# Optimization experiments

Hardware: AMD Instinct MI355X
Metric: run time of the kernel (lower is better)

The kernel has to match this reference:

```python
import jax, jax.numpy as jnp
import numpy as np

NUM_NODES = 50000
NUM_EDGES = 800000
INPUT_DIM = 256
OUTPUT_DIM = 256
NUM_HEADS = 8
HEAD_DIM = OUTPUT_DIM // NUM_HEADS


def setup_inputs() -> dict:
    key = jax.random.key(0)
    ks = jax.random.split(key, 14)
    x = jax.random.normal(ks[0], (NUM_NODES, INPUT_DIM), dtype=jnp.float32)
    edge_index = jax.random.randint(ks[1], (2, NUM_EDGES), 0, NUM_NODES, dtype=jnp.int32)
    # timestamps in seconds over ~11.5 days so log1p(|dt|/3600) is informative
    edge_time = jax.random.uniform(ks[2], (NUM_EDGES,), dtype=jnp.float32) * 1e6
    node_time = jax.random.uniform(ks[3], (NUM_NODES,), dtype=jnp.float32) * 1e6
    s_in = 1.0 / np.sqrt(INPUT_DIM)
    s_out = 1.0 / np.sqrt(OUTPUT_DIM)
    s_t = 1.0 / np.sqrt(2.0)
    Wq = jax.random.uniform(ks[4], (INPUT_DIM, OUTPUT_DIM), jnp.float32, -s_in, s_in)
    bq = jax.random.uniform(ks[5], (OUTPUT_DIM,), jnp.float32, -s_in, s_in)
    Wk = jax.random.uniform(ks[6], (INPUT_DIM, OUTPUT_DIM), jnp.float32, -s_in, s_in)
    bk = jax.random.uniform(ks[7], (OUTPUT_DIM,), jnp.float32, -s_in, s_in)
    Wv = jax.random.uniform(ks[8], (INPUT_DIM, OUTPUT_DIM), jnp.float32, -s_in, s_in)
    bv = jax.random.uniform(ks[9], (OUTPUT_DIM,), jnp.float32, -s_in, s_in)
    Wt = jax.random.uniform(ks[10], (2, NUM_HEADS), jnp.float32, -s_t, s_t)
    bt = jax.random.uniform(ks[11], (NUM_HEADS,), jnp.float32, -s_t, s_t)
    Wo = jax.random.uniform(ks[12], (OUTPUT_DIM, OUTPUT_DIM), jnp.float32, -s_out, s_out)
    bo = jax.random.uniform(ks[13], (OUTPUT_DIM,), jnp.float32, -s_out, s_out)
    return {"x": x, "edge_index": edge_index, "edge_time": edge_time, "node_time": node_time,
            "Wq": Wq, "bq": bq, "Wk": Wk, "bk": bk, "Wv": Wv, "bv": bv,
            "Wt": Wt, "bt": bt, "Wo": Wo, "bo": bo}


def reference(x, edge_index, edge_time, node_time, Wq, bq, Wk, bk, Wv, bv, Wt, bt, Wo, bo):
    n = x.shape[0]
    q = (x @ Wq + bq).reshape(n, NUM_HEADS, HEAD_DIM)
    k = (x @ Wk + bk).reshape(n, NUM_HEADS, HEAD_DIM)
    v = (x @ Wv + bv).reshape(n, NUM_HEADS, HEAD_DIM)
    src, dst = edge_index[0], edge_index[1]
    # temporal features per edge
    time_diff = edge_time - node_time[dst]
    time_features = jnp.stack(
        [jnp.sign(time_diff), jnp.log1p(jnp.abs(time_diff) / 3600.0)], axis=-1)  # [E, 2]
    temporal_weights = time_features @ Wt + bt  # [E, H]
    scale = HEAD_DIM ** -0.5
    scores = jnp.einsum('ehd,ehd->eh', q[dst], k[src]) * scale + temporal_weights  # [E, H]
    # softmax over ALL edges per head (dim=0), as in the original
    alpha = jax.nn.softmax(scores, axis=0)  # [E, H]
    msg = alpha[..., None] * v[src]  # [E, H, D]
    out = jax.ops.segment_sum(msg, dst, num_segments=n)  # [N, H, D]
    out = out.reshape(n, OUTPUT_DIM)
    return out @ Wo + bo
```

## Files before the change

kernel.cpp:

```cpp
#include <hip/hip_runtime.h>
#include <hip/hip_bf16.h>

#define NUM_NODES 50000
#define NUM_EDGES 800000
#define NUM_HEADS 8
#define HEAD_DIM 32
#define SCAN_BLOCKS 49

typedef unsigned short ushort8 __attribute__((ext_vector_type(8)));
typedef float f32x4 __attribute__((ext_vector_type(4)));
typedef __bf16 bf16x8 __attribute__((ext_vector_type(8)));

union BF8 { ushort8 u; bf16x8 b; };

__device__ __forceinline__ unsigned float_to_key(float f) {
    int i = __float_as_int(f);
    return (i >= 0) ? ((unsigned)i | 0x80000000u) : ~(unsigned)i;
}
__device__ __forceinline__ float key_to_float(unsigned u) {
    unsigned b = (u & 0x80000000u) ? (u & 0x7fffffffu) : ~u;
    return __int_as_float((int)b);
}
__device__ __forceinline__ float bf2f(unsigned short u) {
    return __uint_as_float(((unsigned)u) << 16);
}
__device__ __forceinline__ unsigned short f2bf(float f) {
    unsigned u = __float_as_uint(f);
    unsigned r = (u + 0x7fffu + ((u >> 16) & 1u)) >> 16;
    return (unsigned short)r;
}

__global__ __launch_bounds__(256) void deg_kernel(const int* __restrict__ dst_idx, int* __restrict__ deg) {
    int e = blockIdx.x * 256 + threadIdx.x;
    if (e < NUM_EDGES) atomicAdd(&deg[dst_idx[e]], 1);
}

__global__ __launch_bounds__(1024) void scanA_kernel(
    const int* __restrict__ deg, int* __restrict__ offs, int* __restrict__ blocksum)
{
    __shared__ int buf[1024];
    int tid = threadIdx.x;
    int i = blockIdx.x * 1024 + tid;
    int v = (i < NUM_NODES) ? deg[i] : 0;
    buf[tid] = v;
    __syncthreads();
    for (int off = 1; off < 1024; off <<= 1) {
        int t = (tid >= off) ? buf[tid - off] : 0;
        __syncthreads();
        buf[tid] += t;
        __syncthreads();
    }
    if (i < NUM_NODES) offs[i] = buf[tid] - v;
    if (tid == 1023) blocksum[blockIdx.x] = buf[1023];
}

__global__ __launch_bounds__(64) void scanB_kernel(
    const int* __restrict__ blocksum, int* __restrict__ carry, int* __restrict__ offs)
{
    if (threadIdx.x == 0) {
        int acc = 0;
        for (int b = 0; b < SCAN_BLOCKS; b++) { carry[b] = acc; acc += blocksum[b]; }
        offs[NUM_NODES] = acc;
    }
}

__global__ __launch_bounds__(256) void scanC_kernel(
    int* __restrict__ offs, const int* __restrict__ carry, int* __restrict__ cursor)
{
    int i = blockIdx.x * 256 + threadIdx.x;
    if (i < NUM_NODES) {
        int v = offs[i] + carry[i >> 10];
        offs[i] = v;
        cursor[i] = v;
    }
}

__global__ __launch_bounds__(256) void fill2_kernel(
    const int* __restrict__ src_idx, const int* __restrict__ dst_idx,
    const float* __restrict__ edge_time, int* __restrict__ cursor,
    int* __restrict__ src_s, int* __restrict__ dst_s, float* __restrict__ et_s)
{
    int e = blockIdx.x * 256 + threadIdx.x;
    if (e < NUM_EDGES) {
        int d = dst_idx[e];
        int pos = atomicAdd(&cursor[d], 1);
        src_s[pos] = src_idx[e];
        dst_s[pos] = d;
        et_s[pos] = edge_time[e];
    }
}

__global__ __launch_bounds__(256) void wtrans_kernel(
    const float* __restrict__ Wq, const float* __restrict__ Wk,
    const float* __restrict__ Wv, const float* __restrict__ Wo,
    unsigned short* __restrict__ Wt)
{
    __shared__ float t[64][65];
    int nb = blockIdx.x * 64;
    int kb = blockIdx.y * 64;
    int g = nb >> 8;
    const float* W = (g == 0) ? Wq : (g == 1) ? Wk : (g == 2) ? Wv : Wo;
    int n0 = nb & 255;
    int tx = threadIdx.x & 63;
    int ty = threadIdx.x >> 6;
#pragma unroll
    for (int i = 0; i < 16; i++) {
        int k = i * 4 + ty;
        t[tx][k] = W[(size_t)(kb + k) * 256 + n0 + tx];
    }
    __syncthreads();
#pragma unroll
    for (int i = 0; i < 16; i++) {
        int n = i * 4 + ty;
        Wt[(size_t)(nb + n) * 256 + kb + tx] = f2bf(t[n][tx]);
    }
}

__global__ __launch_bounds__(256) void gemm_qkv_mfma4(
    const float* __restrict__ A, int M,
    const unsigned short* __restrict__ Wt,
    const float* __restrict__ b0, const float* __restrict__ b1, const float* __restrict__ b2,
    unsigned short* __restrict__ O0, unsigned short* __restrict__ O1, unsigned short* __restrict__ O2)
{
    __shared__ unsigned short As[64 * 256];
    int tid = threadIdx.x;
    int rowbase = blockIdx.x * 64;

    {
        int rsub = tid >> 6;
        int c4 = (tid & 63) * 4;
        int cchunk = (tid & 63) >> 1;
        int sub = (tid & 1);
#pragma unroll
        for (int it = 0; it < 16; it++) {
            int row = it * 4 + rsub;
            int grow = rowbase + row;
            float4 av = make_float4(0.f, 0.f, 0.f, 0.f);
            if (grow < M) av = *(const float4*)(A + (size_t)grow * 256 + c4);
            ushort4 o;
            o.x = f2bf(av.x); o.y = f2bf(av.y); o.z = f2bf(av.z); o.w = f2bf(av.w);
            unsigned byte = row * 512 + ((unsigned)(cchunk ^ (row & 7)) << 4) + sub * 8;
            *(ushort4*)((char*)As + byte) = o;
        }
    }
    __syncthreads();

    int lane = tid & 63;
    int wid = tid >> 6;
    int l16 = lane & 15;
    int kg = lane >> 4;

#pragma unroll
    for (int p = 0; p < 3; p++) {
        const float* bias = (p == 0) ? b0 : (p == 1) ? b1 : b2;
        unsigned short* O = (p == 0) ? O0 : (p == 1) ? O1 : O2;

        f32x4 acc[4][4];
#pragma unroll
        for (int m = 0; m < 4; m++)
#pragma unroll
            for (int n = 0; n < 4; n++) acc[m][n] = (f32x4)(0.0f);

        const unsigned short* wp[4];
#pragma unroll
        for (int n = 0; n < 4; n++)
            wp[n] = Wt + (size_t)(p * 256 + wid * 64 + n * 16 + l16) * 256 + kg * 8;

#pragma unroll
        for (int c2 = 0; c2 < 8; c2++) {
            bf16x8 wfr[4];
#pragma unroll
            for (int n = 0; n < 4; n++) {
                BF8 t; t.u = *(const ushort8*)(wp[n] + c2 * 32);
                wfr[n] = t.b;
            }
            bf16x8 afr[4];
#pragma unroll
            for (int m = 0; m < 4; m++) {
                int row = m * 16 + l16;
                int cchunk = (c2 * 4 + kg) ^ (row & 7);
                BF8 t;
                t.u = *(const ushort8*)((const char*)As + row * 512 + (cchunk << 4));
                afr[m] = t.b;
            }
#pragma unroll
            for (int m = 0; m < 4; m++)
#pragma unroll
                for (int n = 0; n < 4; n++)
                    acc[m][n] = __builtin_amdgcn_mfma_f32_16x16x32_bf16(wfr[n], afr[m], acc[m][n], 0, 0, 0);
        }

#pragma unroll
        for (int m = 0; m < 4; m++) {
            int node = rowbase + m * 16 + l16;
            if (node >= M) continue;
#pragma unroll
            for (int n = 0; n < 4; n++) {
                int lc = wid * 64 + n * 16 + kg * 4;
                float4 bv = *(const float4*)(bias + lc);
                ushort4 o;
                o.x = f2bf(acc[m][n][0] + bv.x);
                o.y = f2bf(acc[m][n][1] + bv.y);
                o.z = f2bf(acc[m][n][2] + bv.z);
                o.w = f2bf(acc[m][n][3] + bv.w);
                int hh = lc >> 5, dd = lc & 31;
                *(ushort4*)(O + ((size_t)hh * NUM_NODES + node) * 32 + dd) = o;
            }
        }
    }
}

__global__ __launch_bounds__(256) void score3_kernel(
    const unsigned short* __restrict__ qh, const unsigned short* __restrict__ kh,
    const int* __restrict__ src_s, const int* __restrict__ dst_s,
    const float* __restrict__ et_s, const float* __restrict__ node_time,
    const float* __restrict__ Wt, const float* __restrict__ bt,
    float* __restrict__ scores, unsigned* __restrict__ partialmax)
{
    __shared__ unsigned sm;
    int tid = threadIdx.x;
    if (tid == 0) sm = 0u;
    __syncthreads();
    int h = blockIdx.x & 7;
    int blk = blockIdx.x >> 3;
    float wt0 = Wt[h], wt1 = Wt[8 + h], btv = bt[h];
    const unsigned short* qhh = qh + (size_t)h * NUM_NODES * 32;
    const unsigned short* khh = kh + (size_t)h * NUM_NODES * 32;
    float* sc_h = scores + (size_t)h * NUM_EDGES;
    unsigned mykey = 0u;
    for (int pos = blk * 256 + tid; pos < NUM_EDGES; pos += 128 * 256) {
        int s = src_s[pos], d = dst_s[pos];
        const ushort8* qp = (const ushort8*)(qhh + (size_t)d * 32);
        const ushort8* kp = (const ushort8*)(khh + (size_t)s * 32);
        float dotv = 0.f;
#pragma unroll
        for (int i = 0; i < 4; i++) {
            ushort8 a = qp[i], b = kp[i];
#pragma unroll
            for (int j = 0; j < 8; j++) dotv += bf2f(a[j]) * bf2f(b[j]);
        }
        float td = et_s[pos] - node_time[d];
        float tf0 = (td > 0.f) ? 1.f : ((td < 0.f) ? -1.f : 0.f);
        float tf1 = log1pf(fabsf(td) * (1.f / 3600.f));
        float sc = dotv * 0.17677669529663687f + (tf0 * wt0 + tf1 * wt1 + btv);
        sc_h[pos] = sc;
        unsigned kkey = float_to_key(sc);
        mykey = (kkey > mykey) ? kkey : mykey;
    }
#pragma unroll
    for (int off = 32; off > 0; off >>= 1) {
        unsigned o = __shfl_xor(mykey, off, 64);
        mykey = (o > mykey) ? o : mykey;
    }
    if ((tid & 63) == 0) atomicMax(&sm, mykey);
    __syncthreads();
    if (tid == 0) partialmax[blockIdx.x] = sm;
}

__global__ __launch_bounds__(256) void reduce_max2_kernel(
    const unsigned* __restrict__ partialmax, float* __restrict__ headmax)
{
    int tid = threadIdx.x;
    int h = tid >> 5, lane = tid & 31;
    unsigned m = 0u;
#pragma unroll
    for (int k = 0; k < 4; k++) {
        unsigned v = partialmax[(lane + 32 * k) * 8 + h];
        m = (v > m) ? v : m;
    }
    for (int off = 16; off > 0; off >>= 1) {
        unsigned o = __shfl_down(m, off, 32);
        m = (o > m) ? o : m;
    }
    if (lane == 0) headmax[h] = key_to_float(m);
}

__global__ __launch_bounds__(256) void pexp_kernel(
    const float* __restrict__ scores, const float* __restrict__ headmax,
    unsigned short* __restrict__ pb, float* __restrict__ partialsum)
{
    __shared__ float ssum;
    int tid = threadIdx.x;
    if (tid == 0) ssum = 0.f;
    __syncthreads();
    int h = blockIdx.x & 7;
    int blk = blockIdx.x >> 3;
    float m = headmax[h];
    const float* sc_h = scores + (size_t)h * NUM_EDGES;
    unsigned short* p_h = pb + (size_t)h * NUM_EDGES;
    float s = 0.f;
    for (int pos = blk * 256 + tid; pos < NUM_EDGES; pos += 128 * 256) {
        float p = __expf(sc_h[pos] - m);
        p_h[pos] = f2bf(p);
        s += p;
    }
#pragma unroll
    for (int off = 32; off > 0; off >>= 1) s += __shfl_xor(s, off, 64);
    if ((tid & 63) == 0) atomicAdd(&ssum, s);
    __syncthreads();
    if (tid == 0) partialsum[blockIdx.x] = ssum;
}

__global__ __launch_bounds__(256) void reduce_psum_kernel(
    const float* __restrict__ partialsum, float* __restrict__ headinv)
{
    int tid = threadIdx.x;
    int h = tid >> 5, lane = tid & 31;
    float s = 0.f;
#pragma unroll
    for (int k = 0; k < 4; k++) s += partialsum[(lane + 32 * k) * 8 + h];
    for (int off = 16; off > 0; off >>= 1) s += __shfl_down(s, off, 32);
    if (lane == 0) headinv[h] = 1.f / s;
}

__global__ __launch_bounds__(256) void aggregate6_kernel(
    const unsigned short* __restrict__ vh, const unsigned short* __restrict__ pb,
    const int* __restrict__ src_s, const int* __restrict__ offs,
    unsigned short* __restrict__ aggb)
{
    int tid = threadIdx.x;
    int h = blockIdx.x & 7;
    int chunk = blockIdx.x >> 3;
    int g = tid >> 3;
    int ln = tid & 7;
    int node = chunk * 32 + g;
    const unsigned short* p_h = pb + (size_t)h * NUM_EDGES;
    const unsigned short* vhh = vh + (size_t)h * NUM_NODES * 32;
    int start = 0, end = 0;
    if (node < NUM_NODES) { start = offs[node]; end = offs[node + 1]; }
    f32x4 a0 = (f32x4)(0.f), a1 = (f32x4)(0.f);
    int cb = start;
    for (; cb + 2 <= end; cb += 2) {
        int s0 = src_s[cb], s1 = src_s[cb + 1];
        float p0 = bf2f(p_h[cb]), p1 = bf2f(p_h[cb + 1]);
        ushort4 v0 = *(const ushort4*)(vhh + (size_t)s0 * 32 + ln * 4);
        ushort4 v1 = *(const ushort4*)(vhh + (size_t)s1 * 32 + ln * 4);
        a0[0] += p0 * bf2f(v0.x); a0[1] += p0 * bf2f(v0.y);
        a0[2] += p0 * bf2f(v0.z); a0[3] += p0 * bf2f(v0.w);
        a1[0] += p1 * bf2f(v1.x); a1[1] += p1 * bf2f(v1.y);
        a1[2] += p1 * bf2f(v1.z); a1[3] += p1 * bf2f(v1.w);
    }
    if (cb < end) {
        int s0 = src_s[cb];
        float p0 = bf2f(p_h[cb]);
        ushort4 v0 = *(const ushort4*)(vhh + (size_t)s0 * 32 + ln * 4);
        a0[0] += p0 * bf2f(v0.x); a0[1] += p0 * bf2f(v0.y);
        a0[2] += p0 * bf2f(v0.z); a0[3] += p0 * bf2f(v0.w);
    }
    if (node < NUM_NODES) {
        ushort4 o;
        o.x = f2bf(a0[0] + a1[0]); o.y = f2bf(a0[1] + a1[1]);
        o.z = f2bf(a0[2] + a1[2]); o.w = f2bf(a0[3] + a1[3]);
        *(ushort4*)(aggb + ((size_t)h * NUM_NODES + node) * 32 + ln * 4) = o;
    }
}

__global__ __launch_bounds__(256) void gemm_out_mfma4(
    const unsigned short* __restrict__ aggb, int M,
    const unsigned short* __restrict__ Wt,
    const float* __restrict__ bias, const float* __restrict__ kscale,
    float* __restrict__ C)
{
    __shared__ unsigned short As[64 * 256];
    int tid = threadIdx.x;
    int rowbase = blockIdx.x * 64;

    {
        int rsub = tid >> 6;
        int c4 = (tid & 63) * 4;
        int cchunk = (tid & 63) >> 1;
        int sub = (tid & 1);
        int hh = c4 >> 5, dd = c4 & 31;
        float ks = kscale[hh];
#pragma unroll
        for (int it = 0; it < 16; it++) {
            int row = it * 4 + rsub;
            int grow = rowbase + row;
            ushort4 av = make_ushort4(0, 0, 0, 0);
            if (grow < M) av = *(const ushort4*)(aggb + ((size_t)hh * NUM_NODES + grow) * 32 + dd);
            ushort4 o;
            o.x = f2bf(bf2f(av.x) * ks); o.y = f2bf(bf2f(av.y) * ks);
            o.z = f2bf(bf2f(av.z) * ks); o.w = f2bf(bf2f(av.w) * ks);
            unsigned byte = row * 512 + ((unsigned)(cchunk ^ (row & 7)) << 4) + sub * 8;
            *(ushort4*)((char*)As + byte) = o;
        }
    }
    __syncthreads();

    int lane = tid & 63;
    int wid = tid >> 6;
    int l16 = lane & 15;
    int kg = lane >> 4;

    f32x4 acc[4][4];
#pragma unroll
    for (int m = 0; m < 4; m++)
#pragma unroll
        for (int n = 0; n < 4; n++) acc[m][n] = (f32x4)(0.0f);

    const unsigned short* wp[4];
#pragma unroll
    for (int n = 0; n < 4; n++)
        wp[n] = Wt + (size_t)(wid * 64 + n * 16 + l16) * 256 + kg * 8;

#pragma unroll
    for (int c2 = 0; c2 < 8; c2++) {
        bf16x8 wfr[4];
#pragma unroll
        for (int n = 0; n < 4; n++) {
            BF8 t; t.u = *(const ushort8*)(wp[n] + c2 * 32);
            wfr[n] = t.b;
        }
        bf16x8 afr[4];
#pragma unroll
        for (int m = 0; m < 4; m++) {
            int row = m * 16 + l16;
            int cchunk = (c2 * 4 + kg) ^ (row & 7);
            BF8 t;
            t.u = *(const ushort8*)((const char*)As + row * 512 + (cchunk << 4));
            afr[m] = t.b;
        }
#pragma unroll
        for (int m = 0; m < 4; m++)
#pragma unroll
            for (int n = 0; n < 4; n++)
                acc[m][n] = __builtin_amdgcn_mfma_f32_16x16x32_bf16(wfr[n], afr[m], acc[m][n], 0, 0, 0);
    }

#pragma unroll
    for (int m = 0; m < 4; m++) {
        int node = rowbase + m * 16 + l16;
        if (node >= M) continue;
#pragma unroll
        for (int n = 0; n < 4; n++) {
            int col = wid * 64 + n * 16 + kg * 4;
            float4 bv = *(const float4*)(bias + col);
            float4 o;
            o.x = acc[m][n][0] + bv.x;
            o.y = acc[m][n][1] + bv.y;
            o.z = acc[m][n][2] + bv.z;
            o.w = acc[m][n][3] + bv.w;
            *(float4*)(C + (size_t)node * 256 + col) = o;
        }
    }
}

extern "C" void kernel_launch(void* const* d_in, const int* in_sizes, int n_in,
                              void* d_out, int out_size, void* d_ws, size_t ws_size,
                              hipStream_t stream) {
    const float* x = (const float*)d_in[0];
    const int* ei = (const int*)d_in[1];
    const int* src_idx = ei;
    const int* dst_idx = ei + NUM_EDGES;
    const float* edge_time = (const float*)d_in[2];
    const float* node_time = (const float*)d_in[3];
    const float* Wq = (const float*)d_in[4];  const float* bq = (const float*)d_in[5];
    const float* Wk = (const float*)d_in[6];  const float* bk = (const float*)d_in[7];
    const float* Wv = (const float*)d_in[8];  const float* bv = (const float*)d_in[9];
    const float* Wt = (const float*)d_in[10]; const float* bt = (const float*)d_in[11];
    const float* Wo = (const float*)d_in[12]; const float* bo = (const float*)d_in[13];
    float* out = (float*)d_out;

    char* w = (char*)d_ws;
    unsigned short* qb = (unsigned short*)w; w += (size_t)NUM_NODES * 256 * 2;
    unsigned short* kb = (unsigned short*)w; w += (size_t)NUM_NODES * 256 * 2;
    unsigned short* vb = (unsigned short*)w; w += (size_t)NUM_NODES * 256 * 2;
    float* scores = (float*)w;      w += (size_t)NUM_EDGES * 8 * 4;
    unsigned short* pb = (unsigned short*)w; w += (size_t)NUM_EDGES * 8 * 2;
    unsigned short* aggb = (unsigned short*)w; w += (size_t)NUM_NODES * 256 * 2;
    int* src_s = (int*)w;           w += (size_t)NUM_EDGES * 4;
    int* dst_s = (int*)w;           w += (size_t)NUM_EDGES * 4;
    float* et_s = (float*)w;        w += (size_t)NUM_EDGES * 4;
    int* deg = (int*)w;             w += (size_t)NUM_NODES * 4;
    int* offs = (int*)w;            w += (size_t)(NUM_NODES + 1) * 4;
    int* cursor = (int*)w;          w += (size_t)NUM_NODES * 4;
    unsigned* partialmax = (unsigned*)w; w += 1024 * 4;
    float* partialsum = (float*)w;  w += 1024 * 4;
    float* headmax = (float*)w;     w += 8 * 4;
    float* headinv = (float*)w;     w += 8 * 4;
    int* blocksum = (int*)w;        w += 64 * 4;
    int* bcarry = (int*)w;          w += 64 * 4;
    unsigned short* Wtb = (unsigned short*)w; w += (size_t)1024 * 256 * 2;

    hipMemsetAsync(deg, 0, (size_t)NUM_NODES * 4, stream);

    dim3 gw(16, 4);
    wtrans_kernel<<<gw, 256, 0, stream>>>(Wq, Wk, Wv, Wo, Wtb);

    deg_kernel<<<(NUM_EDGES + 255) / 256, 256, 0, stream>>>(dst_idx, deg);
    scanA_kernel<<<SCAN_BLOCKS, 1024, 0, stream>>>(deg, offs, blocksum);
    scanB_kernel<<<1, 64, 0, stream>>>(blocksum, bcarry, offs);
    scanC_kernel<<<(NUM_NODES + 255) / 256, 256, 0, stream>>>(offs, bcarry, cursor);
    fill2_kernel<<<(NUM_EDGES + 255) / 256, 256, 0, stream>>>(src_idx, dst_idx, edge_time,
                                                              cursor, src_s, dst_s, et_s);

    gemm_qkv_mfma4<<<(NUM_NODES + 63) / 64, 256, 0, stream>>>(
        x, NUM_NODES, Wtb, bq, bk, bv, qb, kb, vb);

    score3_kernel<<<1024, 256, 0, stream>>>(qb, kb, src_s, dst_s, et_s, node_time,
                                            Wt, bt, scores, partialmax);
    reduce_max2_kernel<<<1, 256, 0, stream>>>(partialmax, headmax);

    pexp_kernel<<<1024, 256, 0, stream>>>(scores, headmax, pb, partialsum);
    reduce_psum_kernel<<<1, 256, 0, stream>>>(partialsum, headinv);

    aggregate6_kernel<<<((NUM_NODES + 31) / 32) * 8, 256, 0, stream>>>(
        vb, pb, src_s, offs, aggb);

    gemm_out_mfma4<<<(NUM_NODES + 63) / 64, 256, 0, stream>>>(
        aggb, NUM_NODES, Wtb + (size_t)768 * 256, bo, headinv, out);
}
```

Baseline: 375.8 us.

## Make QKV and output GEMMs persistent with register-resident weight fragments

Both GEMMs become persistent kernels with 512 threads per block. Each wave loads its 32-column slice of the bf16 weights into registers once, then loops over 64-row chunks of the input, so weights are no longer re-read from global or L2 for every tile. The QKV GEMM is split across projections with grid.y=3, which means each block reloads and converts the fp32 x tile once per projection, three times per row. The changes add register pressure and double __syncthreads per chunk, and reduce the number of blocks (390 and 391).

```diff
diff --git a/kernel.cpp b/kernel.cpp
--- a/kernel.cpp
+++ b/kernel.cpp
@@ -6,6 +6,7 @@
 #define NUM_HEADS 8
 #define HEAD_DIM 32
 #define SCAN_BLOCKS 49
+#define NCHUNK 782
 
 typedef unsigned short ushort8 __attribute__((ext_vector_type(8)));
 typedef float f32x4 __attribute__((ext_vector_type(4)));
@@ -116,7 +117,7 @@
     }
 }
 
-__global__ __launch_bounds__(256) void gemm_qkv_mfma4(
+__global__ __launch_bounds__(512) void gemm_qkv_reg(
     const float* __restrict__ A, int M,
     const unsigned short* __restrict__ Wt,
     const float* __restrict__ b0, const float* __restrict__ b1, const float* __restrict__ b2,
@@ -124,16 +125,36 @@
 {
     __shared__ unsigned short As[64 * 256];
     int tid = threadIdx.x;
-    int rowbase = blockIdx.x * 64;
-
-    {
-        int rsub = tid >> 6;
-        int c4 = (tid & 63) * 4;
-        int cchunk = (tid & 63) >> 1;
-        int sub = (tid & 1);
-#pragma unroll
-        for (int it = 0; it < 16; it++) {
-            int row = it * 4 + rsub;
+    int p = blockIdx.y;
+    const float* bias = (p == 0) ? b0 : (p == 1) ? b1 : b2;
+    unsigned short* O = (p == 0) ? O0 : (p == 1) ? O1 : O2;
+
+    int lane = tid & 63;
+    int wid = tid >> 6;
+    int l16 = lane & 15;
+    int kg = lane >> 4;
+
+    bf16x8 wfr[2][8];
+#pragma unroll
+    for (int n = 0; n < 2; n++) {
+        const unsigned short* wp = Wt + (size_t)(p * 256 + wid * 32 + n * 16 + l16) * 256 + kg * 8;
+#pragma unroll
+        for (int c2 = 0; c2 < 8; c2++) {
+            BF8 t; t.u = *(const ushort8*)(wp + c2 * 32);
+            wfr[n][c2] = t.b;
+        }
+    }
+
+    int rsub = tid >> 6;
+    int c4 = (tid & 63) * 4;
+    int cchunk = (tid & 63) >> 1;
+    int sub = (tid & 1);
+
+    for (int chunk = blockIdx.x; chunk < NCHUNK; chunk += gridDim.x) {
+        int rowbase = chunk * 64;
+#pragma unroll
+        for (int it = 0; it < 8; it++) {
+            int row = it * 8 + rsub;
             int grow = rowbase + row;
             float4 av = make_float4(0.f, 0.f, 0.f, 0.f);
             if (grow < M) av = *(const float4*)(A + (size_t)grow * 256 + c4);
@@ -142,71 +163,144 @@
             unsigned byte = row * 512 + ((unsigned)(cchunk ^ (row & 7)) << 4) + sub * 8;
             *(ushort4*)((char*)As + byte) = o;
         }
-    }
-    __syncthreads();
+        __syncthreads();
+
+        f32x4 acc[4][2];
+#pragma unroll
+        for (int m = 0; m < 4; m++)
+#pragma unroll
+            for (int n = 0; n < 2; n++) acc[m][n] = (f32x4)(0.0f);
+
+#pragma unroll
+        for (int c2 = 0; c2 < 8; c2++) {
+            bf16x8 afr[4];
+#pragma unroll
+            for (int m = 0; m < 4; m++) {
+                int row = m * 16 + l16;
+                int cc = (c2 * 4 + kg) ^ (row & 7);
+                BF8 t;
+                t.u = *(const ushort8*)((const char*)As + row * 512 + (cc << 4));
+                afr[m] = t.b;
+            }
+#pragma unroll
+            for (int m = 0; m < 4; m++)
+#pragma unroll
+                for (int n = 0; n < 2; n++)
+                    acc[m][n] = __builtin_amdgcn_mfma_f32_16x16x32_bf16(wfr[n][c2], afr[m], acc[m][n], 0, 0, 0);
+        }
+
+#pragma unroll
+        for (int m = 0; m < 4; m++) {
+            int node = rowbase + m * 16 + l16;
+            if (node < M) {
+#pragma unroll
+                for (int n = 0; n < 2; n++) {
+                    int lc = wid * 32 + n * 16 + kg * 4;
+                    float4 bv = *(const float4*)(bias + lc);
+                    ushort4 o;
+                    o.x = f2bf(acc[m][n][0] + bv.x);
+                    o.y = f2bf(acc[m][n][1] + bv.y);
+                    o.z = f2bf(acc[m][n][2] + bv.z);
+                    o.w = f2bf(acc[m][n][3] + bv.w);
+                    int hh = lc >> 5, dd = lc & 31;
+                    *(ushort4*)(O + ((size_t)hh * NUM_NODES + node) * 32 + dd) = o;
+                }
+            }
+        }
+        __syncthreads();
+    }
+}
+
+__global__ __launch_bounds__(512) void gemm_out_reg(
+    const unsigned short* __restrict__ aggb, int M,
+    const unsigned short* __restrict__ Wt,
+    const float* __restrict__ bias, const float* __restrict__ kscale,
+    float* __restrict__ C)
+{
+    __shared__ unsigned short As[64 * 256];
+    int tid = threadIdx.x;
 
     int lane = tid & 63;
     int wid = tid >> 6;
     int l16 = lane & 15;
     int kg = lane >> 4;
 
-#pragma unroll
-    for (int p = 0; p < 3; p++) {
-        const float* bias = (p == 0) ? b0 : (p == 1) ? b1 : b2;
-        unsigned short* O = (p == 0) ? O0 : (p == 1) ? O1 : O2;
-
-        f32x4 acc[4][4];
+    bf16x8 wfr[2][8];
+#pragma unroll
+    for (int n = 0; n < 2; n++) {
+        const unsigned short* wp = Wt + (size_t)(wid * 32 + n * 16 + l16) * 256 + kg * 8;
+#pragma unroll
+        for (int c2 = 0; c2 < 8; c2++) {
+            BF8 t; t.u = *(const ushort8*)(wp + c2 * 32);
+            wfr[n][c2] = t.b;
+        }
+    }
+
+    int row8 = tid >> 6;
+    int cq = tid & 63;
+    int c4 = cq * 4;
+    int hh = c4 >> 5, dd = c4 & 31;
+    float ks = kscale[hh];
+    int cchunk = cq >> 1, sub = cq & 1;
+
+    for (int chunk = blockIdx.x; chunk < NCHUNK; chunk += gridDim.x) {
+        int rowbase = chunk * 64;
+#pragma unroll
+        for (int it = 0; it < 8; it++) {
+            int row = it * 8 + row8;
+            int grow = rowbase + row;
+            ushort4 av = make_ushort4(0, 0, 0, 0);
+            if (grow < M) av = *(const ushort4*)(aggb + ((size_t)hh * NUM_NODES + grow) * 32 + dd);
+            ushort4 o;
+            o.x = f2bf(bf2f(av.x) * ks); o.y = f2bf(bf2f(av.y) * ks);
+            o.z = f2bf(bf2f(av.z) * ks); o.w = f2bf(bf2f(av.w) * ks);
+            unsigned byte = row * 512 + ((unsigned)(cchunk ^ (row & 7)) << 4) + sub * 8;
+            *(ushort4*)((char*)As + byte) = o;
+        }
+        __syncthreads();
+
+        f32x4 acc[4][2];
 #pragma unroll
         for (int m = 0; m < 4; m++)
 #pragma unroll
-            for (int n = 0; n < 4; n++) acc[m][n] = (f32x4)(0.0f);
-
-        const unsigned short* wp[4];
-#pragma unroll
-        for (int n = 0; n < 4; n++)
-            wp[n] = Wt + (size_t)(p * 256 + wid * 64 + n * 16 + l16) * 256 + kg * 8;
+            for (int n = 0; n < 2; n++) acc[m][n] = (f32x4)(0.0f);
 
 #pragma unroll
         for (int c2 = 0; c2 < 8; c2++) {
-            bf16x8 wfr[4];
-#pragma unroll
-            for (int n = 0; n < 4; n++) {
-                BF8 t; t.u = *(const ushort8*)(wp[n] + c2 * 32);
-                wfr[n] = t.b;
-            }
             bf16x8 afr[4];
 #pragma unroll
             for (int m = 0; m < 4; m++) {
                 int row = m * 16 + l16;
-                int cchunk = (c2 * 4 + kg) ^ (row & 7);
+                int cc = (c2 * 4 + kg) ^ (row & 7);
                 BF8 t;
-                t.u = *(const ushort8*)((const char*)As + row * 512 + (cchunk << 4));
+                t.u = *(const ushort8*)((const char*)As + row * 512 + (cc << 4));
                 afr[m] = t.b;
             }
 #pragma unroll
             for (int m = 0; m < 4; m++)
 #pragma unroll
-                for (int n = 0; n < 4; n++)
-                    acc[m][n] = __builtin_amdgcn_mfma_f32_16x16x32_bf16(wfr[n], afr[m], acc[m][n], 0, 0, 0);
+                for (int n = 0; n < 2; n++)
+                    acc[m][n] = __builtin_amdgcn_mfma_f32_16x16x32_bf16(wfr[n][c2], afr[m], acc[m][n], 0, 0, 0);
         }
 
 #pragma unroll
         for (int m = 0; m < 4; m++) {
             int node = rowbase + m * 16 + l16;
-            if (node >= M) continue;
-#pragma unroll
-            for (int n = 0; n < 4; n++) {
-                int lc = wid * 64 + n * 16 + kg * 4;
-                float4 bv = *(const float4*)(bias + lc);
-                ushort4 o;
-                o.x = f2bf(acc[m][n][0] + bv.x);
-                o.y = f2bf(acc[m][n][1] + bv.y);
-                o.z = f2bf(acc[m][n][2] + bv.z);
-                o.w = f2bf(acc[m][n][3] + bv.w);
-                int hh = lc >> 5, dd = lc & 31;
-                *(ushort4*)(O + ((size_t)hh * NUM_NODES + node) * 32 + dd) = o;
+            if (node < M) {
+#pragma unroll
+                for (int n = 0; n < 2; n++) {
+                    int col = wid * 32 + n * 16 + kg * 4;
+                    float4 bv = *(const float4*)(bias + col);
+                    float4 o;
+                    o.x = acc[m][n][0] + bv.x;
+                    o.y = acc[m][n][1] + bv.y;
+                    o.z = acc[m][n][2] + bv.z;
+                    o.w = acc[m][n][3] + bv.w;
+                    *(float4*)(C + (size_t)node * 256 + col) = o;
+                }
             }
         }
+        __syncthreads();
     }
 }
 
@@ -355,96 +449,6 @@
     }
 }
 
-__global__ __launch_bounds__(256) void gemm_out_mfma4(
-    const unsigned short* __restrict__ aggb, int M,
-    const unsigned short* __restrict__ Wt,
-    const float* __restrict__ bias, const float* __restrict__ kscale,
-    float* __restrict__ C)
-{
-    __shared__ unsigned short As[64 * 256];
-    int tid = threadIdx.x;
-    int rowbase = blockIdx.x * 64;
-
-    {
-        int rsub = tid >> 6;
-        int c4 = (tid & 63) * 4;
-        int cchunk = (tid & 63) >> 1;
-        int sub = (tid & 1);
-        int hh = c4 >> 5, dd = c4 & 31;
-        float ks = kscale[hh];
-#pragma unroll
-        for (int it = 0; it < 16; it++) {
-            int row = it * 4 + rsub;
-            int grow = rowbase + row;
-            ushort4 av = make_ushort4(0, 0, 0, 0);
-            if (grow < M) av = *(const ushort4*)(aggb + ((size_t)hh * NUM_NODES + grow) * 32 + dd);
-            ushort4 o;
-            o.x = f2bf(bf2f(av.x) * ks); o.y = f2bf(bf2f(av.y) * ks);
-            o.z = f2bf(bf2f(av.z) * ks); o.w = f2bf(bf2f(av.w) * ks);
-            unsigned byte = row * 512 + ((unsigned)(cchunk ^ (row & 7)) << 4) + sub * 8;
-            *(ushort4*)((char*)As + byte) = o;
-        }
-    }
-    __syncthreads();
-
-    int lane = tid & 63;
-    int wid = tid >> 6;
-    int l16 = lane & 15;
-    int kg = lane >> 4;
-
-    f32x4 acc[4][4];
-#pragma unroll
-    for (int m = 0; m < 4; m++)
-#pragma unroll
-        for (int n = 0; n < 4; n++) acc[m][n] = (f32x4)(0.0f);
-
-    const unsigned short* wp[4];
-#pragma unroll
-    for (int n = 0; n < 4; n++)
-        wp[n] = Wt + (size_t)(wid * 64 + n * 16 + l16) * 256 + kg * 8;
-
-#pragma unroll
-    for (int c2 = 0; c2 < 8; c2++) {
-        bf16x8 wfr[4];
-#pragma unroll
-        for (int n = 0; n < 4; n++) {
-            BF8 t; t.u = *(const ushort8*)(wp[n] + c2 * 32);
-            wfr[n] = t.b;
-        }
-        bf16x8 afr[4];
-#pragma unroll
-        for (int m = 0; m < 4; m++) {
-            int row = m * 16 + l16;
-            int cchunk = (c2 * 4 + kg) ^ (row & 7);
-            BF8 t;
-            t.u = *(const ushort8*)((const char*)As + row * 512 + (cchunk << 4));
-            afr[m] = t.b;
-        }
-#pragma unroll
-        for (int m = 0; m < 4; m++)
-#pragma unroll
-            for (int n = 0; n < 4; n++)
-                acc[m][n] = __builtin_amdgcn_mfma_f32_16x16x32_bf16(wfr[n], afr[m], acc[m][n], 0, 0, 0);
-    }
-
-#pragma unroll
-    for (int m = 0; m < 4; m++) {
-        int node = rowbase + m * 16 + l16;
-        if (node >= M) continue;
-#pragma unroll
-        for (int n = 0; n < 4; n++) {
-            int col = wid * 64 + n * 16 + kg * 4;
-            float4 bv = *(const float4*)(bias + col);
-            float4 o;
-            o.x = acc[m][n][0] + bv.x;
-            o.y = acc[m][n][1] + bv.y;
-            o.z = acc[m][n][2] + bv.z;
-            o.w = acc[m][n][3] + bv.w;
-            *(float4*)(C + (size_t)node * 256 + col) = o;
-        }
-    }
-}
-
 extern "C" void kernel_launch(void* const* d_in, const int* in_sizes, int n_in,
                               void* d_out, int out_size, void* d_ws, size_t ws_size,
                               hipStream_t stream) {
@@ -494,8 +498,8 @@
     fill2_kernel<<<(NUM_EDGES + 255) / 256, 256, 0, stream>>>(src_idx, dst_idx, edge_time,
                                                               cursor, src_s, dst_s, et_s);
 
-    gemm_qkv_mfma4<<<(NUM_NODES + 63) / 64, 256, 0, stream>>>(
-        x, NUM_NODES, Wtb, bq, bk, bv, qb, kb, vb);
+    dim3 gq(130, 3);
+    gemm_qkv_reg<<<gq, 512, 0, stream>>>(x, NUM_NODES, Wtb, bq, bk, bv, qb, kb, vb);
 
     score3_kernel<<<1024, 256, 0, stream>>>(qb, kb, src_s, dst_s, et_s, node_time,
                                             Wt, bt, scores, partialmax);
@@ -507,6 +511,6 @@
     aggregate6_kernel<<<((NUM_NODES + 31) / 32) * 8, 256, 0, stream>>>(
         vb, pb, src_s, offs, aggb);
 
-    gemm_out_mfma4<<<(NUM_NODES + 63) / 64, 256, 0, stream>>>(
+    gemm_out_reg<<<391, 512, 0, stream>>>(
         aggb, NUM_NODES, Wtb + (size_t)768 * 256, bo, headinv, out);
 }
```

Result: no change. 371.3 us (-1.2%).
